# Kernel optimization log

Measured on AMD Instinct MI355X. Metric: run time of the kernel, lower is better.

Reference implementation:

```python
import jax, jax.numpy as jnp
import numpy as np
from jax import lax
from jax.scipy.special import logsumexp

B, T, L, K = 4, 512, 96, 64  # batch, sample_size, num_label, segment_max_len
W = K - 1                    # number of non-zero-start segment lengths considered
NEG = -1e30


def setup_inputs() -> dict:
    key = jax.random.key(0)
    k1, k2 = jax.random.split(key)
    segment_score = jax.random.normal(k1, (B, T, T, L), dtype=jnp.float32)
    transitions = jax.random.uniform(k2, (L + 1, L), dtype=jnp.float32)  # row L = BOS
    return {"segment_score": segment_score, "transitions": transitions}


def _log_z(segment_score, transitions):
    dtype = segment_score.dtype
    trans = transitions[:L]   # [Lp, Lc]
    bos = transitions[L]      # [Lc]
    # NOTE: original code stores exp(...) (not log) for frame 0 -- preserved faithfully.
    alpha0 = jnp.zeros((B, T, L), dtype)
    alpha0 = alpha0.at[:, 0, :].set(jnp.exp(segment_score[:, 0, 0, :] + bos[None, :]))

    w = jnp.arange(1, W + 1, dtype=dtype)  # weight (j+1) per window slot
    jidx = jnp.arange(W)

    def step(alpha, t):
        # scores of all segments ending at frame t: [B, T(start), L]
        seg_t = lax.dynamic_slice(segment_score, (0, 0, t, 0), (B, T, 1, L))[:, :, 0, :]
        base = jnp.maximum(t - W, 0)
        m = jnp.minimum(t, W)  # number of valid non-zero-start entries
        # window slot j: start frame = base+1+j, prev alpha frame = base+j, weight = j+1
        seg_win = lax.dynamic_slice(seg_t, (0, base + 1, 0), (B, W, L))      # [B,W,Lc]
        alpha_win = lax.dynamic_slice(alpha, (0, base, 0), (B, W, L))        # [B,W,Lp]
        total = (alpha_win[:, :, :, None]
                 + (seg_win * w[None, :, None])[:, :, None, :]
                 + (trans[None, :, :] * w[:, None, None])[None, :, :, :])    # [B,W,Lp,Lc]
        total = jnp.where(jidx[None, :, None, None] < m, total, NEG)
        # zero-start segment (only when t+1 <= K i.e. t <= W)
        tlen = (t + 1).astype(dtype)
        z = seg_t[:, 0, :] * tlen + bos[None, :] * tlen                       # [B,Lc]
        z = jnp.where(t <= W, z, NEG)
        cat = jnp.concatenate([total.reshape(B, W * L, L), z[:, None, :]], axis=1)
        new = logsumexp(cat, axis=1)                                          # [B,Lc]
        alpha = lax.dynamic_update_slice(alpha, new[:, None, :], (0, t, 0))
        return alpha, None

    alpha, _ = lax.scan(step, alpha0, jnp.arange(1, T))
    return logsumexp(alpha[:, T - 1, :], axis=1)  # [B]


def reference(segment_score, transitions):
    return _log_z(segment_score, transitions)
```

## Files before the change

kernel.cpp:

```cpp
#include <hip/hip_runtime.h>


#define Tn 512
#define Ln 96
#define HL 48
#define LSQ (Ln * Ln)
#define Wn 63
#define KCH 8
#define NROLE 32
#define NEGINF (-1e30f)
#define SENT 0x7FC00000u

#define AGENT __HIP_MEMORY_SCOPE_AGENT
#define WG __HIP_MEMORY_SCOPE_WORKGROUP
#define RLX __ATOMIC_RELAXED
#define LDSF() asm volatile("s_waitcnt lgkmcnt(0)" ::: "memory")
#define CBAR() asm volatile("" ::: "memory")
#define SIDX(b, i, t) ((((size_t)(b) * Tn + (i)) * Tn + (t)) * Ln)
#define SLEEPSPIN(COND) \
  while (COND) __builtin_amdgcn_s_sleep(1);

typedef unsigned long long u64;
typedef unsigned int u32;
typedef unsigned short u16;

__device__ __forceinline__ float wsumred(float v) {
#pragma unroll
  for (int m = 32; m >= 1; m >>= 1) v += __shfl_xor(v, m, 64);
  return v;
}
__device__ __forceinline__ u64 pack2(float lo, float hi) {
  return (u64)__float_as_uint(lo) | ((u64)__float_as_uint(hi) << 32);
}
__device__ __forceinline__ u16 tobf16(float x) {
  return (u16)((__float_as_uint(x) + 0x8000u) >> 16);
}
__device__ __forceinline__ float wavemax48(float v) {
  int x;
  x = __builtin_amdgcn_update_dpp(__float_as_int(v), __float_as_int(v), 0xB1,
                                  0xF, 0xF, false);
  v = fmaxf(v, __int_as_float(x));
  x = __builtin_amdgcn_update_dpp(__float_as_int(v), __float_as_int(v), 0x4E,
                                  0xF, 0xF, false);
  v = fmaxf(v, __int_as_float(x));
  x = __builtin_amdgcn_update_dpp(__float_as_int(v), __float_as_int(v), 0x141,
                                  0xF, 0xF, false);
  v = fmaxf(v, __int_as_float(x));
  x = __builtin_amdgcn_update_dpp(__float_as_int(v), __float_as_int(v), 0x140,
                                  0xF, 0xF, false);
  v = fmaxf(v, __int_as_float(x));
  float r0 = __int_as_float(__builtin_amdgcn_readlane(__float_as_int(v), 0));
  float r1 = __int_as_float(__builtin_amdgcn_readlane(__float_as_int(v), 16));
  float r2 = __int_as_float(__builtin_amdgcn_readlane(__float_as_int(v), 32));
  float r3 = __int_as_float(__builtin_amdgcn_readlane(__float_as_int(v), 48));
  return fmaxf(fmaxf(r0, r1), fmaxf(r2, r3));
}
__device__ __forceinline__ float comb(float Slo, float Shi, float C0, float C1,
                                      float wseg) {
  const float Cm = fmaxf(C0, C1);
  return Cm + wseg + __logf(__expf(C0 - Cm) * Slo + __expf(C1 - Cm) * Shi);
}

#define MV1(SRC, RR, SLO, SHI)                                       \
  float SLO, SHI;                                                    \
  {                                                                  \
    const float4* A4 = (const float4*)(SRC);                         \
    float a0 = 0, a1 = 0, a2 = 0, a3 = 0;                            \
    _Pragma("unroll") for (int q = 0; q < 12; ++q) {                 \
      float4 a = A4[q];                                              \
      a0 = fmaf(a.x, RR[4 * q + 0], a0);                             \
      a1 = fmaf(a.y, RR[4 * q + 1], a1);                             \
      a2 = fmaf(a.z, RR[4 * q + 2], a2);                             \
      a3 = fmaf(a.w, RR[4 * q + 3], a3);                             \
    }                                                                \
    SLO = (a0 + a1) + (a2 + a3);                                     \
    float b0 = 0, b1 = 0, b2 = 0, b3 = 0;                            \
    _Pragma("unroll") for (int q = 12; q < 24; ++q) {                \
      float4 a = A4[q];                                              \
      b0 = fmaf(a.x, RR[4 * q + 0], b0);                             \
      b1 = fmaf(a.y, RR[4 * q + 1], b1);                             \
      b2 = fmaf(a.z, RR[4 * q + 2], b2);                             \
      b3 = fmaf(a.w, RR[4 * q + 3], b3);                             \
    }                                                                \
    SHI = (b0 + b1) + (b2 + b3);                                     \
  }

#define MVB(SRC, RR, SLO, SHI)                                               \
  float SLO, SHI;                                                            \
  {                                                                          \
    const uint4* A4 = (const uint4*)(SRC);                                   \
    float a0 = 0, a1 = 0, a2 = 0, a3 = 0;                                    \
    _Pragma("unroll") for (int q = 0; q < 6; ++q) {                          \
      uint4 a = A4[q];                                                       \
      a0 = fmaf(__uint_as_float(a.x << 16), RR[8 * q + 0], a0);              \
      a1 = fmaf(__uint_as_float(a.x & 0xFFFF0000u), RR[8 * q + 1], a1);      \
      a2 = fmaf(__uint_as_float(a.y << 16), RR[8 * q + 2], a2);              \
      a3 = fmaf(__uint_as_float(a.y & 0xFFFF0000u), RR[8 * q + 3], a3);      \
      a0 = fmaf(__uint_as_float(a.z << 16), RR[8 * q + 4], a0);              \
      a1 = fmaf(__uint_as_float(a.z & 0xFFFF0000u), RR[8 * q + 5], a1);      \
      a2 = fmaf(__uint_as_float(a.w << 16), RR[8 * q + 6], a2);              \
      a3 = fmaf(__uint_as_float(a.w & 0xFFFF0000u), RR[8 * q + 7], a3);      \
    }                                                                        \
    SLO = (a0 + a1) + (a2 + a3);                                             \
    float b0 = 0, b1 = 0, b2 = 0, b3 = 0;                                    \
    _Pragma("unroll") for (int q = 6; q < 12; ++q) {                         \
      uint4 a = A4[q];                                                       \
      b0 = fmaf(__uint_as_float(a.x << 16), RR[8 * q + 0], b0);              \
      b1 = fmaf(__uint_as_float(a.x & 0xFFFF0000u), RR[8 * q + 1], b1);      \
      b2 = fmaf(__uint_as_float(a.y << 16), RR[8 * q + 2], b2);              \
      b3 = fmaf(__uint_as_float(a.y & 0xFFFF0000u), RR[8 * q + 3], b3);      \
      b0 = fmaf(__uint_as_float(a.z << 16), RR[8 * q + 4], b0);              \
      b1 = fmaf(__uint_as_float(a.z & 0xFFFF0000u), RR[8 * q + 5], b1);      \
      b2 = fmaf(__uint_as_float(a.w << 16), RR[8 * q + 6], b2);              \
      b3 = fmaf(__uint_as_float(a.w & 0xFFFF0000u), RR[8 * q + 7], b3);      \
    }                                                                        \
    SHI = (b0 + b1) + (b2 + b3);                                             \
  }

__global__ void init_ws(u64* ws) {
  const size_t n1 = (size_t)4 * Tn * Ln;
  const size_t n = n1 * 9;
  for (size_t i = (size_t)blockIdx.x * blockDim.x + threadIdx.x; i < n;
       i += (size_t)gridDim.x * blockDim.x)
    ws[i] = (i < n1) ? (((u64)SENT) << 32) : 0ull;
}

__global__ __launch_bounds__(512, 1) void semicrf(
    const float* __restrict__ seg, const float* __restrict__ tr,
    float* __restrict__ out, u64* axp, u64* acc) {
  const int b = blockIdx.x / NROLE;
  const int role = blockIdx.x % NROLE;
  const int tid = threadIdx.x;

  __shared__ __align__(16) float E[LSQ];
  __shared__ __align__(16) u16 AlbRh[8][Ln];
  __shared__ float CRng[8][2];
  __shared__ __align__(16) float slotC2[4][Ln];
  __shared__ float RESTm[4][Ln];
  __shared__ float RESTv[4][Ln];
  __shared__ __align__(16) float Alb_s[4][2][Ln];
  __shared__ float CstS[4][2][2];
  __shared__ float redbuf[2];
  __shared__ int seqA[2], sp2[2][2], rq[2], rfl[2];
  __shared__ int stg[4][2];

  if (tid < 2) { seqA[tid] = -1; rq[tid] = -1; rfl[tid] = -1; }
  if (tid < 4) sp2[tid >> 1][tid & 1] = -1;
  if (tid < 8) stg[tid >> 1][tid & 1] = -1;
  for (int i = tid; i < LSQ; i += 512) E[i] = __expf(tr[i]);
  __syncthreads();

  if (role != 0) {
    const int pair = tid >> 7;
    const int tp = tid & 127;
    const int wv = tp >> 6;
    const int rl = tp & 63;
    const bool act = rl < HL;
    const int lab = wv * HL + (act ? rl : HL - 1);
    const int pu = (role - 1) * 4 + pair;
    if (pu >= 122) return;
    const int d = 3 + (pu >> 1);
    const int par = pu & 1;
    const int j = d & 7;
    u64* chain = acc + (size_t)(j * 4 + b) * Tn * Ln;
    const u64* axB = axp + (size_t)b * Tn * Ln;
    float R[Ln];
#pragma unroll
    for (int lp = 0; lp < Ln; ++lp) R[lp] = E[lp * Ln + lab];
    int wc = 1;
    const bool aHead = (d + KCH > Wn);
    const int t0 = d + (((d ^ par) & 1) ? 1 : 0);

    for (int t = t0; t < Tn; t += 2) {
      const int s = t - d;
      const int w = (t <= Wn) ? (s + 1) : (64 - d);
      while (w > wc) {
        ++wc;
#pragma unroll
        for (int lp = 0; lp < Ln; ++lp) R[lp] *= E[lp * Ln + lab];
      }
      const float segv = seg[SIDX(b, s + 1, t) + lab];
      const size_t tIdx = (size_t)t * Ln + lab;
      const bool head = aHead || (s < KCH);
      u64 ua = 0;
      if (!head) ua = __hip_atomic_load(&chain[tIdx], RLX, AGENT);

      u64 up = __hip_atomic_load(&axB[(size_t)s * Ln + lab], RLX, AGENT);
      while ((u32)(up >> 32) == SENT)
        up = __hip_atomic_load(&axB[(size_t)s * Ln + lab], RLX, AGENT);

      const int buf = (t >> 1) & 1;
      if (act) Alb_s[pair][buf][lab] = __uint_as_float((u32)up);
      if (rl == 0) CstS[pair][buf][wv] = __uint_as_float((u32)(up >> 32));
      LDSF();
      __hip_atomic_store(&stg[pair][wv], t, RLX, WG);
      while (__hip_atomic_load(&stg[pair][wv ^ 1], RLX, WG) < t) {}
      CBAR();
      const float C0 = CstS[pair][buf][0], C1 = CstS[pair][buf][1];
      MV1(Alb_s[pair][buf], R, Slo, Shi)
      const float c = comb(Slo, Shi, C0, C1, (float)w * segv);

      float m, v;
      if (head) {
        m = c;
        v = 1.f;
      } else {
        while (((ua >> 32) & 0xFFu) != (u32)(d + KCH))
          ua = __hip_atomic_load(&chain[tIdx], RLX, AGENT);
        const float pm = __uint_as_float((u32)ua);
        const float pv = __uint_as_float(((u32)(ua >> 32)) & ~0xFFu);
        const float nm = fmaxf(pm, c);
        v = pv * __expf(pm - nm) + __expf(c - nm);
        m = nm;
      }
      if (act) {
        const u32 vb = (__float_as_uint(v) & ~0xFFu) | (u32)d;
        __hip_atomic_store(&chain[tIdx],
                           (u64)__float_as_uint(m) | ((u64)vb << 32), RLX,
                           AGENT);
      }
    }
    return;
  }

  const int w6 = tid >> 6;
  const int l = tid & 63;
  const bool act = l < HL;

  if (w6 < 2) {
    const int h = w6;
    const int lab = h * HL + (act ? l : HL - 1);
    u64* axpB = axp + (size_t)b * Tn * Ln;
    float R1[Ln];
#pragma unroll
    for (int lp = 0; lp < Ln; ++lp) R1[lp] = E[lp * Ln + lab];
    int w1c = 1;
    {
      const float bos = tr[LSQ + lab];
      const float a0 = __expf(seg[SIDX(b, 0, 0) + lab] + bos);
      const float Cw = wavemax48(act ? a0 : NEGINF);
      const float ax0 = __expf(a0 - Cw);
      if (act) AlbRh[0][lab] = tobf16(ax0);
      if (l == 0) CRng[0][h] = Cw;
      LDSF();
      __hip_atomic_store(&seqA[h], 0, RLX, WG);
      if (act) __hip_atomic_store(&axpB[lab], pack2(ax0, Cw), RLX, AGENT);
    }
    float s1q0 = seg[SIDX(b, 1, 1) + lab];
    float s1q1 = seg[SIDX(b, 2, 2) + lab];

    for (int t = 1; t < Tn; ++t) {
      const int s = t - 1;
      const float s1 = s1q0;
      s1q0 = s1q1;
      if (t + 2 < Tn) s1q1 = seg[SIDX(b, t + 2, t + 2) + lab];
      const int w1 = (t <= Wn) ? t : Wn;
      if (w1 > w1c) {
        w1c = w1;
#pragma unroll
        for (int lp = 0; lp < Ln; ++lp) R1[lp] *= E[lp * Ln + lab];
      }
      while (__hip_atomic_load(&seqA[h ^ 1], RLX, WG) < s) {}
      CBAR();
      const float C0 = CRng[s & 7][0], C1 = CRng[s & 7][1];
      MVB(AlbRh[s & 7], R1, Slo, Shi)
      const float c1 = comb(Slo, Shi, C0, C1, (float)w1 * s1);
      float c2 = NEGINF;
      if (t >= 2) {
        while (__hip_atomic_load(&sp2[t & 1][h], RLX, WG) < t) {}
        CBAR();
        c2 = slotC2[t & 3][lab];
      }
      while (__hip_atomic_load(&rq[h], RLX, WG) < t) {}
      CBAR();
      const float mr = RESTm[t & 3][lab], vr = RESTv[t & 3][lab];
      const float M = fmaxf(fmaxf(c1, c2), mr);
      const float vs = __expf(c1 - M) + __expf(c2 - M) + vr * __expf(mr - M);
      const float alpha = M + __logf(vs);
      const float Cw = wavemax48(act ? alpha : NEGINF);
      const float axn = __expf(alpha - Cw);
      if (act) AlbRh[t & 7][lab] = tobf16(axn);
      if (l == 0) CRng[t & 7][h] = Cw;
      LDSF();
      __hip_atomic_store(&seqA[h], t, RLX, WG);
      if (act)
        __hip_atomic_store(&axpB[(size_t)t * Ln + lab], pack2(axn, Cw), RLX,
                           AGENT);
      if (t == Tn - 1) {
        const float sm = wsumred(act ? axn : 0.f);
        const float Gw = Cw + __logf(sm);
        if (l == 0) redbuf[h] = Gw;
        LDSF();
        __hip_atomic_store(&rfl[h], 1, RLX, WG);
        if (h == 0 && l == 0) {
          while (__hip_atomic_load(&rfl[1], RLX, WG) < 1) {}
          CBAR();
          const float G0 = redbuf[0], G1 = redbuf[1];
          const float Mx = fmaxf(G0, G1);
          out[b] = Mx + __logf(__expf(G0 - Mx) + __expf(G1 - Mx));
        }
      }
    }
    return;
  }

  if (w6 < 6) {
    const int p = (w6 - 2) >> 1;
    const int h = (w6 - 2) & 1;
    const int lab = h * HL + (act ? l : HL - 1);
    float R[Ln];
#pragma unroll
    for (int lp = 0; lp < Ln; ++lp) R[lp] = E[lp * Ln + lab];
    int wc = 1;
    const int t0 = 2 + p;
    float q0 = seg[SIDX(b, t0 - 1, t0) + lab];
    float q1 = (t0 + 2 < Tn) ? seg[SIDX(b, t0 + 1, t0 + 2) + lab] : 0.f;

    for (int t = t0; t < Tn; t += 2) {
      const int s = t - 2;
      const int w = (t <= Wn) ? (s + 1) : 62;
      const float segv = q0;
      q0 = q1;
      if (t + 4 < Tn) q1 = seg[SIDX(b, t + 3, t + 4) + lab];
      while (w > wc) {
        ++wc;
#pragma unroll
        for (int lp = 0; lp < Ln; ++lp) R[lp] *= E[lp * Ln + lab];
      }
      SLEEPSPIN(__hip_atomic_load(&seqA[0], RLX, WG) < s ||
                __hip_atomic_load(&seqA[1], RLX, WG) < s)
      CBAR();
      const float C0 = CRng[s & 7][0], C1 = CRng[s & 7][1];
      MVB(AlbRh[s & 7], R, Slo, Shi)
      const float c = comb(Slo, Shi, C0, C1, (float)w * segv);
      if (act) slotC2[t & 3][lab] = c;
      LDSF();
      __hip_atomic_store(&sp2[p][h], t, RLX, WG);
    }
    return;
  }

  {
    const int h = w6 - 6;
    const int lab = h * HL + (act ? l : HL - 1);
    const float bos = tr[LSQ + lab];
    const int endd[8] = {8, 9, 10, 3, 4, 5, 6, 7};
    float zq0 = seg[SIDX(b, 0, 1) + lab];
    float zq1 = seg[SIDX(b, 0, 2) + lab];
    u64 u[8];
#pragma unroll
    for (int jj = 0; jj < 8; ++jj) u[jj] = 0;

    for (int t = 1; t < Tn; ++t) {
      const float szv = zq0;
      zq0 = zq1;
      if (t + 2 <= Wn) zq1 = seg[SIDX(b, 0, t + 2) + lab];

      float em[8], ev[8];
#pragma unroll
      for (int jj = 0; jj < 8; ++jj) {
        if (t >= endd[jj]) {
          const size_t aIdx = (((size_t)jj * 4 + b) * Tn + t) * Ln + lab;
          while (((u[jj] >> 32) & 0xFFu) != (u32)endd[jj])
            u[jj] = __hip_atomic_load(&acc[aIdx], RLX, AGENT);
          em[jj] = __uint_as_float((u32)u[jj]);
          ev[jj] = __uint_as_float(((u32)(u[jj] >> 32)) & ~0xFFu);
        } else {
          em[jj] = NEGINF;
          ev[jj] = 0.f;
        }
      }
      const float zv = (t <= Wn) ? (float)(t + 1) * (szv + bos) : NEGINF;

      float M = zv;
#pragma unroll
      for (int jj = 0; jj < 8; ++jj) M = fmaxf(M, em[jj]);
      float vs = __expf(zv - M);
#pragma unroll
      for (int jj = 0; jj < 8; ++jj) vs += ev[jj] * __expf(em[jj] - M);

      if (act) {
        RESTm[t & 3][lab] = M;
        RESTv[t & 3][lab] = vs;
      }
      LDSF();
      __hip_atomic_store(&rq[h], t, RLX, WG);

      const int tn = t + 1;
      if (tn < Tn) {
#pragma unroll
        for (int jj = 0; jj < 8; ++jj)
          if (tn >= endd[jj])
            u[jj] = __hip_atomic_load(
                &acc[(((size_t)jj * 4 + b) * Tn + tn) * Ln + lab], RLX, AGENT);
      }
    }
    return;
  }
}

extern "C" void kernel_launch(void* const* d_in, const int* in_sizes, int n_in,
                              void* d_out, int out_size, void* d_ws,
                              size_t ws_size, hipStream_t stream) {
  const float* seg = (const float*)d_in[0];
  const float* tr = (const float*)d_in[1];
  float* out = (float*)d_out;

  u64* axp = (u64*)d_ws;
  u64* acc = axp + (size_t)4 * Tn * Ln;

  hipLaunchKernelGGL(init_ws, dim3(2048), dim3(256), 0, stream, (u64*)d_ws);
  hipLaunchKernelGGL(semicrf, dim3(4 * NROLE), dim3(512), 0, stream, seg, tr,
                     out, axp, acc);
}
```

Baseline: 819.1 us.

## Move distance-2 segments to remote role blocks and split REST aggregation by parity

Distance-2 segment contributions no longer come from dedicated in-block waves. They are now computed by the remote role blocks, which start at d=2 instead of 3 and so use all 124 pair units. The local aggregator waves become two parity-split REST waves that handle alternate timesteps, each prefetching their chain slots two steps ahead. The main alpha waves now wait on one flag per step instead of two, and write the global alpha before the LDS copy so remote consumers see it earlier. The cost is that chain j=2 now depends on a cross-block global round trip that sits right on the critical path.

```diff
diff --git a/kernel.cpp b/kernel.cpp
--- a/kernel.cpp
+++ b/kernel.cpp
@@ -17,8 +17,6 @@
 #define LDSF() asm volatile("s_waitcnt lgkmcnt(0)" ::: "memory")
 #define CBAR() asm volatile("" ::: "memory")
 #define SIDX(b, i, t) ((((size_t)(b) * Tn + (i)) * Tn + (t)) * Ln)
-#define SLEEPSPIN(COND) \
-  while (COND) __builtin_amdgcn_s_sleep(1);
 
 typedef unsigned long long u64;
 typedef unsigned int u32;
@@ -135,17 +133,16 @@
   __shared__ __align__(16) float E[LSQ];
   __shared__ __align__(16) u16 AlbRh[8][Ln];
   __shared__ float CRng[8][2];
-  __shared__ __align__(16) float slotC2[4][Ln];
   __shared__ float RESTm[4][Ln];
   __shared__ float RESTv[4][Ln];
   __shared__ __align__(16) float Alb_s[4][2][Ln];
   __shared__ float CstS[4][2][2];
   __shared__ float redbuf[2];
-  __shared__ int seqA[2], sp2[2][2], rq[2], rfl[2];
+  __shared__ int seqA[2], rq[2][2], rfl[2];
   __shared__ int stg[4][2];
 
-  if (tid < 2) { seqA[tid] = -1; rq[tid] = -1; rfl[tid] = -1; }
-  if (tid < 4) sp2[tid >> 1][tid & 1] = -1;
+  if (tid < 2) { seqA[tid] = -1; rfl[tid] = -1; }
+  if (tid < 4) rq[tid >> 1][tid & 1] = -1;
   if (tid < 8) stg[tid >> 1][tid & 1] = -1;
   for (int i = tid; i < LSQ; i += 512) E[i] = __expf(tr[i]);
   __syncthreads();
@@ -158,8 +155,7 @@
     const bool act = rl < HL;
     const int lab = wv * HL + (act ? rl : HL - 1);
     const int pu = (role - 1) * 4 + pair;
-    if (pu >= 122) return;
-    const int d = 3 + (pu >> 1);
+    const int d = 2 + (pu >> 1);
     const int par = pu & 1;
     const int j = d & 7;
     u64* chain = acc + (size_t)(j * 4 + b) * Tn * Ln;
@@ -226,6 +222,7 @@
   const int w6 = tid >> 6;
   const int l = tid & 63;
   const bool act = l < HL;
+  if (w6 >= 6) return;
 
   if (w6 < 2) {
     const int h = w6;
@@ -240,11 +237,11 @@
       const float a0 = __expf(seg[SIDX(b, 0, 0) + lab] + bos);
       const float Cw = wavemax48(act ? a0 : NEGINF);
       const float ax0 = __expf(a0 - Cw);
+      if (act) __hip_atomic_store(&axpB[lab], pack2(ax0, Cw), RLX, AGENT);
       if (act) AlbRh[0][lab] = tobf16(ax0);
       if (l == 0) CRng[0][h] = Cw;
       LDSF();
       __hip_atomic_store(&seqA[h], 0, RLX, WG);
-      if (act) __hip_atomic_store(&axpB[lab], pack2(ax0, Cw), RLX, AGENT);
     }
     float s1q0 = seg[SIDX(b, 1, 1) + lab];
     float s1q1 = seg[SIDX(b, 2, 2) + lab];
@@ -265,27 +262,21 @@
       const float C0 = CRng[s & 7][0], C1 = CRng[s & 7][1];
       MVB(AlbRh[s & 7], R1, Slo, Shi)
       const float c1 = comb(Slo, Shi, C0, C1, (float)w1 * s1);
-      float c2 = NEGINF;
-      if (t >= 2) {
-        while (__hip_atomic_load(&sp2[t & 1][h], RLX, WG) < t) {}
-        CBAR();
-        c2 = slotC2[t & 3][lab];
-      }
-      while (__hip_atomic_load(&rq[h], RLX, WG) < t) {}
+      while (__hip_atomic_load(&rq[t & 1][h], RLX, WG) < t) {}
       CBAR();
       const float mr = RESTm[t & 3][lab], vr = RESTv[t & 3][lab];
-      const float M = fmaxf(fmaxf(c1, c2), mr);
-      const float vs = __expf(c1 - M) + __expf(c2 - M) + vr * __expf(mr - M);
+      const float M = fmaxf(c1, mr);
+      const float vs = __expf(c1 - M) + vr * __expf(mr - M);
       const float alpha = M + __logf(vs);
       const float Cw = wavemax48(act ? alpha : NEGINF);
       const float axn = __expf(alpha - Cw);
+      if (act)
+        __hip_atomic_store(&axpB[(size_t)t * Ln + lab], pack2(axn, Cw), RLX,
+                           AGENT);
       if (act) AlbRh[t & 7][lab] = tobf16(axn);
       if (l == 0) CRng[t & 7][h] = Cw;
       LDSF();
       __hip_atomic_store(&seqA[h], t, RLX, WG);
-      if (act)
-        __hip_atomic_store(&axpB[(size_t)t * Ln + lab], pack2(axn, Cw), RLX,
-                           AGENT);
       if (t == Tn - 1) {
         const float sm = wsumred(act ? axn : 0.f);
         const float Gw = Cw + __logf(sm);
@@ -304,77 +295,67 @@
     return;
   }
 
-  if (w6 < 6) {
+  {
     const int p = (w6 - 2) >> 1;
     const int h = (w6 - 2) & 1;
     const int lab = h * HL + (act ? l : HL - 1);
-    float R[Ln];
-#pragma unroll
-    for (int lp = 0; lp < Ln; ++lp) R[lp] = E[lp * Ln + lab];
-    int wc = 1;
-    const int t0 = 2 + p;
-    float q0 = seg[SIDX(b, t0 - 1, t0) + lab];
-    float q1 = (t0 + 2 < Tn) ? seg[SIDX(b, t0 + 1, t0 + 2) + lab] : 0.f;
+    const float bos = tr[LSQ + lab];
+    const int endd[8] = {8, 9, 2, 3, 4, 5, 6, 7};
+    const int t0 = (p == 1) ? 1 : 2;
+    float zq0 = (t0 <= Wn) ? seg[SIDX(b, 0, t0) + lab] : 0.f;
+    float zq1 = (t0 + 2 <= Wn) ? seg[SIDX(b, 0, t0 + 2) + lab] : 0.f;
+    u64 u[8];
+#pragma unroll
+    for (int jj = 0; jj < 8; ++jj) {
+      u[jj] = 0;
+      if (jj != 2 && jj != 3 && t0 >= endd[jj])
+        u[jj] = __hip_atomic_load(
+            &acc[(((size_t)jj * 4 + b) * Tn + t0) * Ln + lab], RLX, AGENT);
+    }
 
     for (int t = t0; t < Tn; t += 2) {
-      const int s = t - 2;
-      const int w = (t <= Wn) ? (s + 1) : 62;
-      const float segv = q0;
-      q0 = q1;
-      if (t + 4 < Tn) q1 = seg[SIDX(b, t + 3, t + 4) + lab];
-      while (w > wc) {
-        ++wc;
-#pragma unroll
-        for (int lp = 0; lp < Ln; ++lp) R[lp] *= E[lp * Ln + lab];
-      }
-      SLEEPSPIN(__hip_atomic_load(&seqA[0], RLX, WG) < s ||
-                __hip_atomic_load(&seqA[1], RLX, WG) < s)
-      CBAR();
-      const float C0 = CRng[s & 7][0], C1 = CRng[s & 7][1];
-      MVB(AlbRh[s & 7], R, Slo, Shi)
-      const float c = comb(Slo, Shi, C0, C1, (float)w * segv);
-      if (act) slotC2[t & 3][lab] = c;
-      LDSF();
-      __hip_atomic_store(&sp2[p][h], t, RLX, WG);
-    }
-    return;
-  }
-
-  {
-    const int h = w6 - 6;
-    const int lab = h * HL + (act ? l : HL - 1);
-    const float bos = tr[LSQ + lab];
-    const int endd[8] = {8, 9, 10, 3, 4, 5, 6, 7};
-    float zq0 = seg[SIDX(b, 0, 1) + lab];
-    float zq1 = seg[SIDX(b, 0, 2) + lab];
-    u64 u[8];
-#pragma unroll
-    for (int jj = 0; jj < 8; ++jj) u[jj] = 0;
-
-    for (int t = 1; t < Tn; ++t) {
+      if (t >= 2)
+        u[2] = __hip_atomic_load(
+            &acc[(((size_t)2 * 4 + b) * Tn + t) * Ln + lab], RLX, AGENT);
+      if (t >= 3)
+        u[3] = __hip_atomic_load(
+            &acc[(((size_t)3 * 4 + b) * Tn + t) * Ln + lab], RLX, AGENT);
       const float szv = zq0;
       zq0 = zq1;
-      if (t + 2 <= Wn) zq1 = seg[SIDX(b, 0, t + 2) + lab];
-
+      if (t + 4 <= Wn) zq1 = seg[SIDX(b, 0, t + 4) + lab];
+
+      const float zv = (t <= Wn) ? (float)(t + 1) * (szv + bos) : NEGINF;
+      float M = zv;
       float em[8], ev[8];
 #pragma unroll
       for (int jj = 0; jj < 8; ++jj) {
+        if (jj == 2 || jj == 3) continue;
         if (t >= endd[jj]) {
           const size_t aIdx = (((size_t)jj * 4 + b) * Tn + t) * Ln + lab;
           while (((u[jj] >> 32) & 0xFFu) != (u32)endd[jj])
             u[jj] = __hip_atomic_load(&acc[aIdx], RLX, AGENT);
           em[jj] = __uint_as_float((u32)u[jj]);
           ev[jj] = __uint_as_float(((u32)(u[jj] >> 32)) & ~0xFFu);
+          M = fmaxf(M, em[jj]);
         } else {
           em[jj] = NEGINF;
           ev[jj] = 0.f;
         }
       }
-      const float zv = (t <= Wn) ? (float)(t + 1) * (szv + bos) : NEGINF;
-
-      float M = zv;
-#pragma unroll
-      for (int jj = 0; jj < 8; ++jj) M = fmaxf(M, em[jj]);
+#pragma unroll
+      for (int jj = 2; jj <= 3; ++jj) {
+        if (t >= endd[jj]) {
+          const size_t aIdx = (((size_t)jj * 4 + b) * Tn + t) * Ln + lab;
+          while (((u[jj] >> 32) & 0xFFu) != (u32)endd[jj])
+            u[jj] = __hip_atomic_load(&acc[aIdx], RLX, AGENT);
+          em[jj] = __uint_as_float((u32)u[jj]);
+          ev[jj] = __uint_as_float(((u32)(u[jj] >> 32)) & ~0xFFu);
+          M = fmaxf(M, em[jj]);
+        } else {
+          em[jj] = NEGINF;
+          ev[jj] = 0.f;
+        }
+      }
       float vs = __expf(zv - M);
 #pragma unroll
       for (int jj = 0; jj < 8; ++jj) vs += ev[jj] * __expf(em[jj] - M);
@@ -384,13 +365,13 @@
         RESTv[t & 3][lab] = vs;
       }
       LDSF();
-      __hip_atomic_store(&rq[h], t, RLX, WG);
-
-      const int tn = t + 1;
+      __hip_atomic_store(&rq[p][h], t, RLX, WG);
+
+      const int tn = t + 2;
       if (tn < Tn) {
 #pragma unroll
         for (int jj = 0; jj < 8; ++jj)
-          if (tn >= endd[jj])
+          if (jj != 2 && jj != 3 && tn >= endd[jj])
             u[jj] = __hip_atomic_load(
                 &acc[(((size_t)jj * 4 + b) * Tn + tn) * Ln + lab], RLX, AGENT);
       }
```

New measurement: 862.0 us. 5.2% more time.

## Move segment length 3 into the main workgroup and unroll the critical loop by two

Applied to the files above, without the earlier changes.

The in-block helper waves now split by segment length: one pair computes length-2 contributions and a new pair computes length-3 contributions into slotC3. The remote chain roles start at length 4, so the role count drops from 32 to 31 and the previous role cap is removed. The critical wave loop and the rest-reducer are unrolled two steps per iteration with deeper seg prefetch. Sleep-spins become busy-waits, and the global alpha store moves ahead of the LDS publish. The aim is to shorten per-step latency on the serial alpha chain, at the cost of more LDS handshakes and more register pressure.

```diff
diff --git a/kernel.cpp b/kernel.cpp
--- a/kernel.cpp
+++ b/kernel.cpp
@@ -7,7 +7,7 @@
 #define LSQ (Ln * Ln)
 #define Wn 63
 #define KCH 8
-#define NROLE 32
+#define NROLE 31
 #define NEGINF (-1e30f)
 #define SENT 0x7FC00000u
 
@@ -17,8 +17,6 @@
 #define LDSF() asm volatile("s_waitcnt lgkmcnt(0)" ::: "memory")
 #define CBAR() asm volatile("" ::: "memory")
 #define SIDX(b, i, t) ((((size_t)(b) * Tn + (i)) * Tn + (t)) * Ln)
-#define SLEEPSPIN(COND) \
-  while (COND) __builtin_amdgcn_s_sleep(1);
 
 typedef unsigned long long u64;
 typedef unsigned int u32;
@@ -136,16 +134,22 @@
   __shared__ __align__(16) u16 AlbRh[8][Ln];
   __shared__ float CRng[8][2];
   __shared__ __align__(16) float slotC2[4][Ln];
+  __shared__ __align__(16) float slotC3[4][Ln];
   __shared__ float RESTm[4][Ln];
   __shared__ float RESTv[4][Ln];
   __shared__ __align__(16) float Alb_s[4][2][Ln];
   __shared__ float CstS[4][2][2];
   __shared__ float redbuf[2];
-  __shared__ int seqA[2], sp2[2][2], rq[2], rfl[2];
+  __shared__ int seqH[2], sp2[2], sp3[2], rq[2], rfl[2];
   __shared__ int stg[4][2];
 
-  if (tid < 2) { seqA[tid] = -1; rq[tid] = -1; rfl[tid] = -1; }
-  if (tid < 4) sp2[tid >> 1][tid & 1] = -1;
+  if (tid < 2) {
+    seqH[tid] = -1;
+    sp2[tid] = -1;
+    sp3[tid] = -1;
+    rq[tid] = -1;
+    rfl[tid] = -1;
+  }
   if (tid < 8) stg[tid >> 1][tid & 1] = -1;
   for (int i = tid; i < LSQ; i += 512) E[i] = __expf(tr[i]);
   __syncthreads();
@@ -158,8 +162,7 @@
     const bool act = rl < HL;
     const int lab = wv * HL + (act ? rl : HL - 1);
     const int pu = (role - 1) * 4 + pair;
-    if (pu >= 122) return;
-    const int d = 3 + (pu >> 1);
+    const int d = 4 + (pu >> 1);
     const int par = pu & 1;
     const int j = d & 7;
     u64* chain = acc + (size_t)(j * 4 + b) * Tn * Ln;
@@ -240,55 +243,67 @@
       const float a0 = __expf(seg[SIDX(b, 0, 0) + lab] + bos);
       const float Cw = wavemax48(act ? a0 : NEGINF);
       const float ax0 = __expf(a0 - Cw);
+      if (act) __hip_atomic_store(&axpB[lab], pack2(ax0, Cw), RLX, AGENT);
       if (act) AlbRh[0][lab] = tobf16(ax0);
       if (l == 0) CRng[0][h] = Cw;
       LDSF();
-      __hip_atomic_store(&seqA[h], 0, RLX, WG);
-      if (act) __hip_atomic_store(&axpB[lab], pack2(ax0, Cw), RLX, AGENT);
-    }
-    float s1q0 = seg[SIDX(b, 1, 1) + lab];
-    float s1q1 = seg[SIDX(b, 2, 2) + lab];
-
-    for (int t = 1; t < Tn; ++t) {
-      const int s = t - 1;
-      const float s1 = s1q0;
-      s1q0 = s1q1;
-      if (t + 2 < Tn) s1q1 = seg[SIDX(b, t + 2, t + 2) + lab];
-      const int w1 = (t <= Wn) ? t : Wn;
+      __hip_atomic_store(&seqH[h], 0, RLX, WG);
+    }
+    float qa = seg[SIDX(b, 1, 1) + lab];
+    float qb = seg[SIDX(b, 2, 2) + lab];
+    float qa2 = seg[SIDX(b, 3, 3) + lab];
+    float qb2 = seg[SIDX(b, 4, 4) + lab];
+
+    for (int k = 0; k < 256; ++k) {
+      const int t1 = 2 * k + 1, t2 = 2 * k + 2;
+      const float s1 = qa, s2 = qb;
+      qa = qa2;
+      qb = qb2;
+      if (t1 + 4 < Tn) qa2 = seg[SIDX(b, t1 + 4, t1 + 4) + lab];
+      if (t2 + 4 < Tn) qb2 = seg[SIDX(b, t2 + 4, t2 + 4) + lab];
+
+      const int w1 = (t1 <= Wn) ? t1 : Wn;
       if (w1 > w1c) {
         w1c = w1;
 #pragma unroll
         for (int lp = 0; lp < Ln; ++lp) R1[lp] *= E[lp * Ln + lab];
       }
-      while (__hip_atomic_load(&seqA[h ^ 1], RLX, WG) < s) {}
+      while (__hip_atomic_load(&seqH[h ^ 1], RLX, WG) < t1 - 1) {}
       CBAR();
-      const float C0 = CRng[s & 7][0], C1 = CRng[s & 7][1];
-      MVB(AlbRh[s & 7], R1, Slo, Shi)
-      const float c1 = comb(Slo, Shi, C0, C1, (float)w1 * s1);
-      float c2 = NEGINF;
-      if (t >= 2) {
-        while (__hip_atomic_load(&sp2[t & 1][h], RLX, WG) < t) {}
-        CBAR();
-        c2 = slotC2[t & 3][lab];
-      }
-      while (__hip_atomic_load(&rq[h], RLX, WG) < t) {}
+      const float C0a = CRng[(t1 - 1) & 7][0], C1a = CRng[(t1 - 1) & 7][1];
+      MVB(AlbRh[(t1 - 1) & 7], R1, SloA, ShiA)
+      const float c1a = comb(SloA, ShiA, C0a, C1a, (float)w1 * s1);
+      float c2a = NEGINF, c3a = NEGINF;
+      if (t1 >= 2) {
+        while (__hip_atomic_load(&sp2[h], RLX, WG) < t1) {}
+        CBAR();
+        c2a = slotC2[t1 & 3][lab];
+      }
+      if (t1 >= 3) {
+        while (__hip_atomic_load(&sp3[h], RLX, WG) < t1) {}
+        CBAR();
+        c3a = slotC3[t1 & 3][lab];
+      }
+      while (__hip_atomic_load(&rq[h], RLX, WG) < t1) {}
       CBAR();
-      const float mr = RESTm[t & 3][lab], vr = RESTv[t & 3][lab];
-      const float M = fmaxf(fmaxf(c1, c2), mr);
-      const float vs = __expf(c1 - M) + __expf(c2 - M) + vr * __expf(mr - M);
-      const float alpha = M + __logf(vs);
-      const float Cw = wavemax48(act ? alpha : NEGINF);
-      const float axn = __expf(alpha - Cw);
-      if (act) AlbRh[t & 7][lab] = tobf16(axn);
-      if (l == 0) CRng[t & 7][h] = Cw;
+      const float mra = RESTm[t1 & 3][lab], vra = RESTv[t1 & 3][lab];
+      const float Ma = fmaxf(fmaxf(c1a, c2a), fmaxf(c3a, mra));
+      const float vsa = __expf(c1a - Ma) + __expf(c2a - Ma) +
+                        __expf(c3a - Ma) + vra * __expf(mra - Ma);
+      const float alpha1 = Ma + __logf(vsa);
+      const float Cw1 = wavemax48(act ? alpha1 : NEGINF);
+      const float ax1 = __expf(alpha1 - Cw1);
+      if (act)
+        __hip_atomic_store(&axpB[(size_t)t1 * Ln + lab], pack2(ax1, Cw1), RLX,
+                           AGENT);
+      if (act) AlbRh[t1 & 7][lab] = tobf16(ax1);
+      if (l == 0) CRng[t1 & 7][h] = Cw1;
       LDSF();
-      __hip_atomic_store(&seqA[h], t, RLX, WG);
-      if (act)
-        __hip_atomic_store(&axpB[(size_t)t * Ln + lab], pack2(axn, Cw), RLX,
-                           AGENT);
-      if (t == Tn - 1) {
-        const float sm = wsumred(act ? axn : 0.f);
-        const float Gw = Cw + __logf(sm);
+      __hip_atomic_store(&seqH[h], t1, RLX, WG);
+
+      if (t1 == Tn - 1) {
+        const float sm = wsumred(act ? ax1 : 0.f);
+        const float Gw = Cw1 + __logf(sm);
         if (l == 0) redbuf[h] = Gw;
         LDSF();
         __hip_atomic_store(&rfl[h], 1, RLX, WG);
@@ -299,43 +314,161 @@
           const float Mx = fmaxf(G0, G1);
           out[b] = Mx + __logf(__expf(G0 - Mx) + __expf(G1 - Mx));
         }
-      }
+        break;
+      }
+
+      const int w2 = (t2 <= Wn) ? t2 : Wn;
+      if (w2 > w1c) {
+        w1c = w2;
+#pragma unroll
+        for (int lp = 0; lp < Ln; ++lp) R1[lp] *= E[lp * Ln + lab];
+      }
+      while (__hip_atomic_load(&seqH[h ^ 1], RLX, WG) < t1) {}
+      CBAR();
+      const float C0b = CRng[t1 & 7][0], C1b = CRng[t1 & 7][1];
+      MVB(AlbRh[t1 & 7], R1, SloB, ShiB)
+      const float c1b = comb(SloB, ShiB, C0b, C1b, (float)w2 * s2);
+      while (__hip_atomic_load(&sp2[h], RLX, WG) < t2) {}
+      CBAR();
+      const float c2b = slotC2[t2 & 3][lab];
+      float c3b = NEGINF;
+      if (t2 >= 3) {
+        while (__hip_atomic_load(&sp3[h], RLX, WG) < t2) {}
+        CBAR();
+        c3b = slotC3[t2 & 3][lab];
+      }
+      while (__hip_atomic_load(&rq[h], RLX, WG) < t2) {}
+      CBAR();
+      const float mrb = RESTm[t2 & 3][lab], vrb = RESTv[t2 & 3][lab];
+      const float Mb = fmaxf(fmaxf(c1b, c2b), fmaxf(c3b, mrb));
+      const float vsb = __expf(c1b - Mb) + __expf(c2b - Mb) +
+                        __expf(c3b - Mb) + vrb * __expf(mrb - Mb);
+      const float alpha2 = Mb + __logf(vsb);
+      const float Cw2 = wavemax48(act ? alpha2 : NEGINF);
+      const float ax2 = __expf(alpha2 - Cw2);
+      if (act)
+        __hip_atomic_store(&axpB[(size_t)t2 * Ln + lab], pack2(ax2, Cw2), RLX,
+                           AGENT);
+      if (act) AlbRh[t2 & 7][lab] = tobf16(ax2);
+      if (l == 0) CRng[t2 & 7][h] = Cw2;
+      LDSF();
+      __hip_atomic_store(&seqH[h], t2, RLX, WG);
     }
     return;
   }
 
-  if (w6 < 6) {
-    const int p = (w6 - 2) >> 1;
-    const int h = (w6 - 2) & 1;
+  if (w6 < 4) {
+    const int h = w6 - 2;
     const int lab = h * HL + (act ? l : HL - 1);
     float R[Ln];
 #pragma unroll
     for (int lp = 0; lp < Ln; ++lp) R[lp] = E[lp * Ln + lab];
     int wc = 1;
-    const int t0 = 2 + p;
-    float q0 = seg[SIDX(b, t0 - 1, t0) + lab];
-    float q1 = (t0 + 2 < Tn) ? seg[SIDX(b, t0 + 1, t0 + 2) + lab] : 0.f;
-
-    for (int t = t0; t < Tn; t += 2) {
-      const int s = t - 2;
-      const int w = (t <= Wn) ? (s + 1) : 62;
-      const float segv = q0;
-      q0 = q1;
-      if (t + 4 < Tn) q1 = seg[SIDX(b, t + 3, t + 4) + lab];
-      while (w > wc) {
-        ++wc;
-#pragma unroll
-        for (int lp = 0; lp < Ln; ++lp) R[lp] *= E[lp * Ln + lab];
-      }
-      SLEEPSPIN(__hip_atomic_load(&seqA[0], RLX, WG) < s ||
-                __hip_atomic_load(&seqA[1], RLX, WG) < s)
-      CBAR();
-      const float C0 = CRng[s & 7][0], C1 = CRng[s & 7][1];
-      MVB(AlbRh[s & 7], R, Slo, Shi)
-      const float c = comb(Slo, Shi, C0, C1, (float)w * segv);
-      if (act) slotC2[t & 3][lab] = c;
-      LDSF();
-      __hip_atomic_store(&sp2[p][h], t, RLX, WG);
+    float q1 = seg[SIDX(b, 2, 3) + lab];
+    float q2 = seg[SIDX(b, 1, 2) + lab];
+    float q1n = seg[SIDX(b, 4, 5) + lab];
+    float q2n = seg[SIDX(b, 3, 4) + lab];
+
+    for (int k = 0; k < 256; ++k) {
+      const int t1 = 2 * k + 1, t2 = 2 * k + 2;
+      const float sv1 = q1, sv2 = q2;
+      q1 = q1n;
+      q2 = q2n;
+      if (t1 + 4 < Tn) q1n = seg[SIDX(b, t1 + 3, t1 + 4) + lab];
+      if (t2 + 4 < Tn) q2n = seg[SIDX(b, t2 + 3, t2 + 4) + lab];
+
+      if (t1 >= 3) {
+        const int w = (t1 <= Wn) ? (t1 - 1) : 62;
+        if (w > wc) {
+          wc = w;
+#pragma unroll
+          for (int lp = 0; lp < Ln; ++lp) R[lp] *= E[lp * Ln + lab];
+        }
+        while (__hip_atomic_load(&seqH[0], RLX, WG) < t1 - 2 ||
+               __hip_atomic_load(&seqH[1], RLX, WG) < t1 - 2) {}
+        CBAR();
+        const float C0 = CRng[(t1 - 2) & 7][0], C1 = CRng[(t1 - 2) & 7][1];
+        MVB(AlbRh[(t1 - 2) & 7], R, SloA, ShiA)
+        const float c = comb(SloA, ShiA, C0, C1, (float)w * sv1);
+        if (act) slotC2[t1 & 3][lab] = c;
+        LDSF();
+        __hip_atomic_store(&sp2[h], t1, RLX, WG);
+      }
+      if (t2 < Tn) {
+        const int w = (t2 <= Wn) ? (t2 - 1) : 62;
+        if (w > wc) {
+          wc = w;
+#pragma unroll
+          for (int lp = 0; lp < Ln; ++lp) R[lp] *= E[lp * Ln + lab];
+        }
+        while (__hip_atomic_load(&seqH[0], RLX, WG) < t2 - 2 ||
+               __hip_atomic_load(&seqH[1], RLX, WG) < t2 - 2) {}
+        CBAR();
+        const float C0 = CRng[(t2 - 2) & 7][0], C1 = CRng[(t2 - 2) & 7][1];
+        MVB(AlbRh[(t2 - 2) & 7], R, SloB, ShiB)
+        const float c = comb(SloB, ShiB, C0, C1, (float)w * sv2);
+        if (act) slotC2[t2 & 3][lab] = c;
+        LDSF();
+        __hip_atomic_store(&sp2[h], t2, RLX, WG);
+      }
+    }
+    return;
+  }
+
+  if (w6 < 6) {
+    const int h = w6 - 4;
+    const int lab = h * HL + (act ? l : HL - 1);
+    float R[Ln];
+#pragma unroll
+    for (int lp = 0; lp < Ln; ++lp) R[lp] = E[lp * Ln + lab];
+    int wc = 1;
+    float q1 = seg[SIDX(b, 1, 3) + lab];
+    float q2 = seg[SIDX(b, 2, 4) + lab];
+    float q1n = seg[SIDX(b, 3, 5) + lab];
+    float q2n = seg[SIDX(b, 4, 6) + lab];
+
+    for (int k = 0; k < 256; ++k) {
+      const int t1 = 2 * k + 1, t2 = 2 * k + 2;
+      const float sv1 = q1, sv2 = q2;
+      q1 = q1n;
+      q2 = q2n;
+      if (t1 + 4 < Tn) q1n = seg[SIDX(b, t1 + 2, t1 + 4) + lab];
+      if (t2 + 4 < Tn) q2n = seg[SIDX(b, t2 + 2, t2 + 4) + lab];
+
+      if (t1 >= 3) {
+        const int w = (t1 <= Wn) ? (t1 - 2) : 61;
+        if (w > wc) {
+          wc = w;
+#pragma unroll
+          for (int lp = 0; lp < Ln; ++lp) R[lp] *= E[lp * Ln + lab];
+        }
+        while (__hip_atomic_load(&seqH[0], RLX, WG) < t1 - 3 ||
+               __hip_atomic_load(&seqH[1], RLX, WG) < t1 - 3) {}
+        CBAR();
+        const float C0 = CRng[(t1 - 3) & 7][0], C1 = CRng[(t1 - 3) & 7][1];
+        MVB(AlbRh[(t1 - 3) & 7], R, SloA, ShiA)
+        const float c = comb(SloA, ShiA, C0, C1, (float)w * sv1);
+        if (act) slotC3[t1 & 3][lab] = c;
+        LDSF();
+        __hip_atomic_store(&sp3[h], t1, RLX, WG);
+      }
+      if (t2 >= 3 && t2 < Tn) {
+        const int w = (t2 <= Wn) ? (t2 - 2) : 61;
+        if (w > wc) {
+          wc = w;
+#pragma unroll
+          for (int lp = 0; lp < Ln; ++lp) R[lp] *= E[lp * Ln + lab];
+        }
+        while (__hip_atomic_load(&seqH[0], RLX, WG) < t2 - 3 ||
+               __hip_atomic_load(&seqH[1], RLX, WG) < t2 - 3) {}
+        CBAR();
+        const float C0 = CRng[(t2 - 3) & 7][0], C1 = CRng[(t2 - 3) & 7][1];
+        MVB(AlbRh[(t2 - 3) & 7], R, SloB, ShiB)
+        const float c = comb(SloB, ShiB, C0, C1, (float)w * sv2);
+        if (act) slotC3[t2 & 3][lab] = c;
+        LDSF();
+        __hip_atomic_store(&sp3[h], t2, RLX, WG);
+      }
     }
     return;
   }
@@ -344,55 +477,97 @@
     const int h = w6 - 6;
     const int lab = h * HL + (act ? l : HL - 1);
     const float bos = tr[LSQ + lab];
-    const int endd[8] = {8, 9, 10, 3, 4, 5, 6, 7};
-    float zq0 = seg[SIDX(b, 0, 1) + lab];
-    float zq1 = seg[SIDX(b, 0, 2) + lab];
-    u64 u[8];
-#pragma unroll
-    for (int jj = 0; jj < 8; ++jj) u[jj] = 0;
-
-    for (int t = 1; t < Tn; ++t) {
-      const float szv = zq0;
-      zq0 = zq1;
-      if (t + 2 <= Wn) zq1 = seg[SIDX(b, 0, t + 2) + lab];
-
-      float em[8], ev[8];
-#pragma unroll
-      for (int jj = 0; jj < 8; ++jj) {
-        if (t >= endd[jj]) {
-          const size_t aIdx = (((size_t)jj * 4 + b) * Tn + t) * Ln + lab;
-          while (((u[jj] >> 32) & 0xFFu) != (u32)endd[jj])
-            u[jj] = __hip_atomic_load(&acc[aIdx], RLX, AGENT);
-          em[jj] = __uint_as_float((u32)u[jj]);
-          ev[jj] = __uint_as_float(((u32)(u[jj] >> 32)) & ~0xFFu);
-        } else {
-          em[jj] = NEGINF;
-          ev[jj] = 0.f;
-        }
-      }
-      const float zv = (t <= Wn) ? (float)(t + 1) * (szv + bos) : NEGINF;
-
-      float M = zv;
-#pragma unroll
-      for (int jj = 0; jj < 8; ++jj) M = fmaxf(M, em[jj]);
-      float vs = __expf(zv - M);
-#pragma unroll
-      for (int jj = 0; jj < 8; ++jj) vs += ev[jj] * __expf(em[jj] - M);
-
-      if (act) {
-        RESTm[t & 3][lab] = M;
-        RESTv[t & 3][lab] = vs;
-      }
-      LDSF();
-      __hip_atomic_store(&rq[h], t, RLX, WG);
-
-      const int tn = t + 1;
-      if (tn < Tn) {
+    const int endd[8] = {8, 9, 10, 11, 4, 5, 6, 7};
+    float z1 = seg[SIDX(b, 0, 1) + lab];
+    float z2 = seg[SIDX(b, 0, 2) + lab];
+    float z1n = seg[SIDX(b, 0, 3) + lab];
+    float z2n = seg[SIDX(b, 0, 4) + lab];
+    u64 u1[8], u2[8];
+#pragma unroll
+    for (int jj = 0; jj < 8; ++jj) {
+      u1[jj] = 0;
+      u2[jj] = 0;
+    }
+
+    for (int k = 0; k < 256; ++k) {
+      const int t1 = 2 * k + 1, t2 = 2 * k + 2;
+      const float sz1 = z1, sz2 = z2;
+      z1 = z1n;
+      z2 = z2n;
+      if (t1 + 4 <= Wn) z1n = seg[SIDX(b, 0, t1 + 4) + lab];
+      if (t2 + 4 <= Wn) z2n = seg[SIDX(b, 0, t2 + 4) + lab];
+
+      {
+        const float zv = (t1 <= Wn) ? (float)(t1 + 1) * (sz1 + bos) : NEGINF;
+        float M = zv;
+        float em[8], ev[8];
+#pragma unroll
+        for (int jj = 0; jj < 8; ++jj) {
+          if (t1 >= endd[jj]) {
+            const size_t aIdx = (((size_t)jj * 4 + b) * Tn + t1) * Ln + lab;
+            while (((u1[jj] >> 32) & 0xFFu) != (u32)endd[jj])
+              u1[jj] = __hip_atomic_load(&acc[aIdx], RLX, AGENT);
+            em[jj] = __uint_as_float((u32)u1[jj]);
+            ev[jj] = __uint_as_float(((u32)(u1[jj] >> 32)) & ~0xFFu);
+            M = fmaxf(M, em[jj]);
+          } else {
+            em[jj] = NEGINF;
+            ev[jj] = 0.f;
+          }
+        }
+        float vs = __expf(zv - M);
+#pragma unroll
+        for (int jj = 0; jj < 8; ++jj) vs += ev[jj] * __expf(em[jj] - M);
+        if (act) {
+          RESTm[t1 & 3][lab] = M;
+          RESTv[t1 & 3][lab] = vs;
+        }
+        LDSF();
+        __hip_atomic_store(&rq[h], t1, RLX, WG);
+      }
+      if (t2 < Tn) {
+        const float zv = (t2 <= Wn) ? (float)(t2 + 1) * (sz2 + bos) : NEGINF;
+        float M = zv;
+        float em[8], ev[8];
+#pragma unroll
+        for (int jj = 0; jj < 8; ++jj) {
+          if (t2 >= endd[jj]) {
+            const size_t aIdx = (((size_t)jj * 4 + b) * Tn + t2) * Ln + lab;
+            while (((u2[jj] >> 32) & 0xFFu) != (u32)endd[jj])
+              u2[jj] = __hip_atomic_load(&acc[aIdx], RLX, AGENT);
+            em[jj] = __uint_as_float((u32)u2[jj]);
+            ev[jj] = __uint_as_float(((u32)(u2[jj] >> 32)) & ~0xFFu);
+            M = fmaxf(M, em[jj]);
+          } else {
+            em[jj] = NEGINF;
+            ev[jj] = 0.f;
+          }
+        }
+        float vs = __expf(zv - M);
+#pragma unroll
+        for (int jj = 0; jj < 8; ++jj) vs += ev[jj] * __expf(em[jj] - M);
+        if (act) {
+          RESTm[t2 & 3][lab] = M;
+          RESTv[t2 & 3][lab] = vs;
+        }
+        LDSF();
+        __hip_atomic_store(&rq[h], t2, RLX, WG);
+      }
+      if (t1 + 2 < Tn) {
 #pragma unroll
         for (int jj = 0; jj < 8; ++jj)
-          if (tn >= endd[jj])
-            u[jj] = __hip_atomic_load(
-                &acc[(((size_t)jj * 4 + b) * Tn + tn) * Ln + lab], RLX, AGENT);
+          if (t1 + 2 >= endd[jj])
+            u1[jj] = __hip_atomic_load(
+                &acc[(((size_t)jj * 4 + b) * Tn + (t1 + 2)) * Ln + lab], RLX,
+                AGENT);
+      }
+      if (t2 + 2 < Tn) {
+#pragma unroll
+        for (int jj = 0; jj < 8; ++jj)
+          if (t2 + 2 >= endd[jj])
+            u2[jj] = __hip_atomic_load(
+                &acc[(((size_t)jj * 4 + b) * Tn + (t2 + 2)) * Ln + lab], RLX,
+                AGENT);
       }
     }
     return;
```

Result: slower. 857.2 us (+4.7%).
